# Optimization experiments

Hardware: AMD Instinct MI355X
Metric: run time of the kernel (lower is better)

## Reference

```python
import jax, jax.numpy as jnp
import numpy as np

DIM = 512
HEADS = 4
MARGIN = 1.0


def _attn_pool(x, Wq, bq, Wk, bk, Wv, bv, Wo, bo):
    # SelfAttention(video_dim, m_dim=DIM, heads=HEADS) followed by mean over time
    B, T, _ = x.shape
    hd = DIM // HEADS
    q = (x @ Wq + bq).reshape(B, T, HEADS, hd)
    k = (x @ Wk + bk).reshape(B, T, HEADS, hd)
    v = (x @ Wv + bv).reshape(B, T, HEADS, hd)
    a = jax.nn.softmax(jnp.einsum('bthd,bshd->bhts', q, k) / jnp.sqrt(jnp.float32(hd)), axis=-1)
    out = jnp.einsum('bhts,bshd->bthd', a, v).reshape(B, T, DIM) @ Wo + bo
    return out.mean(axis=1)  # [B, DIM]


def _ranking(x1, x2, gmask, margin):
    # vectorized form of the per-row torch.roll loop:
    # s[i, b] = <x1[b], x2[(b - i) mod B]>
    B = x1.shape[0]
    idx = (jnp.arange(B)[None, :] - jnp.arange(B)[:, None]) % B  # [B, B]
    s = jnp.einsum('bc,ibc->ib', x1, x2[idx])                    # [B, B]
    mask = gmask[idx] & gmask[None, :]                           # [B, B]
    # max-margin ranking loss with per-column masked mean, then mean over valid cols
    loss = jnp.maximum(0.0, margin + s[1:] - s[0:1])             # [B-1, B]
    m = mask[1:]
    cnt = m.sum(axis=0)
    col_mean = jnp.where(cnt > 0, (loss * m).sum(axis=0) / jnp.maximum(cnt, 1), 0.0)
    valid = cnt > 0
    loss_val = jnp.sum(col_mean * valid) / jnp.maximum(valid.sum(), 1)
    # ranking accuracy: idx==0 iff the true (row 0) score is max among selected
    sel_sum = jnp.sum(jnp.where(mask, s, 0.0), axis=0)
    col_valid = (sel_sum != 0) & mask.any(axis=0)
    s_masked = jnp.where(mask, s, -jnp.inf)
    top_is_first = (s[0] >= s_masked.max(axis=0)).astype(jnp.float32)
    acc = jnp.sum(jnp.where(col_valid, top_is_first, 0.0)) / jnp.maximum(col_valid.sum(), 1)
    return loss_val, jax.lax.stop_gradient(acc)


def setup_inputs() -> dict:
    key = jax.random.key(0)
    ks = iter(jax.random.split(key, 64))

    def nrm(shape, s=0.02):
        return jax.random.normal(next(ks), shape, jnp.float32) * s

    inp = {
        'o': jax.random.normal(next(ks), (128, 1024, DIM), jnp.float32),
        'rgb': jax.random.normal(next(ks), (128, 64, 2048), jnp.float32),
        'audio': jax.random.normal(next(ks), (128, 64, 128), jnp.float32),
        'group_mask': jax.random.randint(next(ks), (128,), 0, 2).astype(bool),
    }
    for name, d in (('rgb', 2048), ('audio', 128)):
        inp[f'{name}_Wq'] = nrm((d, DIM)); inp[f'{name}_bq'] = jnp.zeros((DIM,), jnp.float32)
        inp[f'{name}_Wk'] = nrm((d, DIM)); inp[f'{name}_bk'] = jnp.zeros((DIM,), jnp.float32)
        inp[f'{name}_Wv'] = nrm((d, DIM)); inp[f'{name}_bv'] = jnp.zeros((DIM,), jnp.float32)
        inp[f'{name}_Wo'] = nrm((DIM, DIM)); inp[f'{name}_bo'] = jnp.zeros((DIM,), jnp.float32)
        inp[f'{name}_W2'] = nrm((DIM, DIM)); inp[f'{name}_b2'] = jnp.zeros((DIM,), jnp.float32)
    inp['expand_W'] = nrm((DIM, 2 * DIM))
    inp['expand_b'] = jnp.zeros((2 * DIM,), jnp.float32)
    return inp


def reference(o, rgb, audio, group_mask,
              rgb_Wq, rgb_bq, rgb_Wk, rgb_bk, rgb_Wv, rgb_bv, rgb_Wo, rgb_bo, rgb_W2, rgb_b2,
              audio_Wq, audio_bq, audio_Wk, audio_bk, audio_Wv, audio_bv, audio_Wo, audio_bo,
              audio_W2, audio_b2, expand_W, expand_b):
    # per-modality encoders (CollaborativeGating multiplies are discarded in the
    # original forward, so gating is a no-op on the output -> skipped)
    f_rgb = _attn_pool(rgb, rgb_Wq, rgb_bq, rgb_Wk, rgb_bk, rgb_Wv, rgb_bv, rgb_Wo, rgb_bo) @ rgb_W2 + rgb_b2
    f_aud = _attn_pool(audio, audio_Wq, audio_bq, audio_Wk, audio_bk, audio_Wv, audio_bv, audio_Wo, audio_bo) @ audio_W2 + audio_b2
    feat = jnp.concatenate([f_rgb, f_aud], axis=-1)  # [B, 2*DIM]
    oo = o.mean(axis=-2) @ expand_W + expand_b       # [B, 2*DIM]
    oo = oo / jnp.maximum(jnp.linalg.norm(oo, axis=-1, keepdims=True), 1e-12)
    l1, a1 = _ranking(oo, feat, group_mask, MARGIN)
    l2, a2 = _ranking(feat, oo, group_mask, MARGIN)
    loss = l1 + l2
    acc = (a1 + a2) / 2.0
    return loss, acc
```

## Files before the change

kernel.cpp:

```cpp
#include <hip/hip_runtime.h>
#include <hip/hip_bf16.h>
#include <math.h>


using bf16x8 = __attribute__((ext_vector_type(8))) __bf16;
using f32x4  = __attribute__((ext_vector_type(4))) float;

enum : size_t {
  B_PART = 0,
  B_OM   = B_PART + (size_t)128*16*2*512*4,
  B_OO   = B_OM   + (size_t)128*512*4,
  B_G    = B_OO   + (size_t)128*1024*4,
  B_PP   = B_G    + (size_t)128*128*4,
  B_PO   = B_PP   + (size_t)2*128*512*4,
  B_FEAT = B_PO   + (size_t)2*128*512*4,
  B_QBF  = B_FEAT + (size_t)2*128*512*4,
  B_KBF  = B_QBF  + (size_t)2*8192*512*2,
  B_VBF  = B_KBF  + (size_t)2*8192*512*2,
  B_XR   = B_VBF  + (size_t)2*8192*512*2,
  B_XA   = B_XR   + (size_t)8192*2048*2,
  B_WT   = B_XA   + (size_t)8192*128*2,
  B_END  = B_WT   + (size_t)3*512*2048*2 + (size_t)3*512*128*2
};

__device__ __forceinline__ unsigned short f2bf(float f) {
  __hip_bfloat16 h = __float2bfloat16(f);
  return __builtin_bit_cast(unsigned short, h);
}
__device__ __forceinline__ unsigned pack2(float a, float b) {
  return (unsigned)f2bf(a) | ((unsigned)f2bf(b) << 16);
}

struct PrepArgs {
  const float* xr; unsigned short* xrb;
  const float* xa; unsigned short* xab;
  const float* w[6];
  unsigned short* wt[6];
};

__device__ __forceinline__ void castT64(const float* __restrict__ W,
                                        unsigned short* __restrict__ Wt,
                                        int K, int n0, int k0, int tid) {
  __shared__ float t[64][65];
  int c = tid & 63, r4 = tid >> 6;
#pragma unroll
  for (int i = 0; i < 16; ++i) {
    int r = r4 * 16 + i;
    t[c][r] = W[(size_t)(k0 + r) * 512 + n0 + c];
  }
  __syncthreads();
  int nr = tid >> 3, kk = (tid & 7) * 8;
#pragma unroll
  for (int p = 0; p < 2; ++p) {
    int n = nr + p * 32;
    float4 x0 = *(const float4*)&t[n][kk];
    float4 x1 = *(const float4*)&t[n][kk + 4];
    uint4 pk;
    pk.x = pack2(x0.x, x0.y); pk.y = pack2(x0.z, x0.w);
    pk.z = pack2(x1.x, x1.y); pk.w = pack2(x1.z, x1.w);
    *(uint4*)&Wt[(size_t)(n0 + n) * K + k0 + kk] = pk;
  }
}

__device__ __forceinline__ void cast8(const float* __restrict__ x,
                                      unsigned short* __restrict__ y,
                                      int i, int stride, int total) {
  for (; i < total; i += stride) {
    float4 v0 = *(const float4*)(x + (size_t)i * 8);
    float4 v1 = *(const float4*)(x + (size_t)i * 8 + 4);
    uint4 pk;
    pk.x = pack2(v0.x, v0.y); pk.y = pack2(v0.z, v0.w);
    pk.z = pack2(v1.x, v1.y); pk.w = pack2(v1.z, v1.w);
    *(uint4*)(y + (size_t)i * 8) = pk;
  }
}

__global__ __launch_bounds__(256) void prep_k(PrepArgs a) {
  int bid = blockIdx.x, tid = threadIdx.x;
  if (bid < 768) {
    int w = bid >> 8, t = bid & 255;
    castT64(a.w[w], a.wt[w], 2048, (t >> 5) * 64, (t & 31) * 64, tid);
  } else if (bid < 816) {
    int t = bid - 768; int w = t >> 4; t &= 15;
    castT64(a.w[3 + w], a.wt[3 + w], 128, (t >> 1) * 64, (t & 1) * 64, tid);
  } else if (bid < 1840) {
    cast8(a.xr, a.xrb, (bid - 816) * 256 + tid, 262144, 2097152);
  } else {
    cast8(a.xa, a.xab, (bid - 1840) * 256 + tid, 16384, 131072);
  }
}

struct QkvAll {
  const unsigned short* A[2];
  const unsigned short* Wt[6];
  const float* bias[6];
  unsigned short* out[6];
  const float* o; float* part;
};

__device__ __forceinline__ void stage16(const void* g, void* l) {
  __builtin_amdgcn_global_load_lds((const __attribute__((address_space(1))) void*)g,
                                   (__attribute__((address_space(3))) void*)l, 16, 0, 0);
}

__global__ __launch_bounds__(256) void qkv_mean_k(QkvAll args) {
  __shared__ __align__(16) char smem[49152];

  int id = blockIdx.x;
  int blk = id / 448, off = id % 448;

  if (off >= 192) {
    int mb = blk * 256 + (off - 192);
    int c = mb & 15, b = mb >> 4;
    const float* base = args.o + ((size_t)b * 1024 + (size_t)c * 64) * 512;
    int tid = threadIdx.x;
    int d4 = (tid & 127) << 2, half = tid >> 7;
    float4 s = {0.f, 0.f, 0.f, 0.f};
    for (int t = half; t < 64; t += 2) {
      float4 v = *(const float4*)(base + (size_t)t * 512 + d4);
      s.x += v.x; s.y += v.y; s.z += v.z; s.w += v.w;
    }
    *(float4*)(args.part + (((size_t)b * 16 + c) * 2 + half) * 512 + d4) = s;
    return;
  }

  int qid = blk * 192 + off;
  int mi = qid >= 768 ? 1 : 0; qid -= mi * 768;
  int by = qid & 63, bx = (qid >> 6) & 3, bz = qid >> 8;
  int K = mi ? 128 : 2048;
  int nt = K >> 5;
  const unsigned short* A = args.A[mi];
  int wi = mi * 3 + bz;
  const unsigned short* Bt = args.Wt[wi];
  const float* bias = args.bias[wi];

  int tid = threadIdx.x;
  int l = tid & 63, w = tid >> 6;
  int row0 = by * 128, col0 = bx * 128;
  int wrow = (w & 1) * 64, wcol = (w >> 1) * 64;
  int kg = l >> 4, lr = l & 15;

  float bv[4];
#pragma unroll
  for (int n = 0; n < 4; ++n) bv[n] = bias[col0 + wcol + n * 16 + lr];
  asm volatile("" :: "v"(bv[0]), "v"(bv[1]), "v"(bv[2]), "v"(bv[3]));

  auto stage_pair = [&](char* dbuf, int k0s) {
#pragma unroll
    for (int i = 0; i < 2; ++i) {
      int c = w * 128 + i * 64 + l;
      int B_ = c << 4;
      int e6 = ((B_ >> 6) ^ (B_ >> 8)) & 1;
      int E  = B_ ^ (e6 << 4) ^ (((B_ >> 7) & 1) << 5) ^ (((B_ >> 8) & 1) << 6);
      int r = E >> 6, s = ((E >> 4) & 3) << 3;
      stage16(A + (size_t)(row0 + r) * K + k0s + s, dbuf + (w * 128 + i * 64) * 16);
      stage16(Bt + (size_t)(col0 + r) * K + k0s + s, dbuf + 8192 + (w * 128 + i * 64) * 16);
    }
  };

  f32x4 acc[4][4] = {};
  int xorA = (lr & 15 & 7) << 4;

  stage_pair(smem, 0);
  if (nt > 1) stage_pair(smem + 16384, 32);
  int cur = 0;
  for (int t = 0; t < nt; ++t) {
    if (t + 1 < nt) {
      asm volatile("s_waitcnt vmcnt(4)" ::: "memory");
    } else {
      asm volatile("s_waitcnt vmcnt(0)" ::: "memory");
    }
    __builtin_amdgcn_s_barrier();
    __builtin_amdgcn_sched_barrier(0);

    if (t + 2 < nt) {
      int nb = cur + 2; if (nb >= 3) nb -= 3;
      stage_pair(smem + nb * 16384, (t + 2) << 5);
    }

    const char* Ab = smem + cur * 16384;
    const char* Bb = Ab + 8192;
    bf16x8 af[4], bfr[4];
#pragma unroll
    for (int m = 0; m < 4; ++m) {
      int ra = wrow + m * 16 + lr;
      int rb = wcol + m * 16 + lr;
      af[m]  = *(const bf16x8*)(Ab + (((ra << 6) + (kg << 4)) ^ xorA));
      bfr[m] = *(const bf16x8*)(Bb + (((rb << 6) + (kg << 4)) ^ xorA));
    }
#pragma unroll
    for (int m = 0; m < 4; ++m)
#pragma unroll
      for (int n = 0; n < 4; ++n)
        acc[m][n] = __builtin_amdgcn_mfma_f32_16x16x32_bf16(af[m], bfr[n], acc[m][n], 0, 0, 0);

    __builtin_amdgcn_sched_barrier(0);
    cur += 1; if (cur >= 3) cur = 0;
  }

  __syncthreads();

  float* cst = (float*)(smem) + w * 1024;
  unsigned short* C = args.out[wi];
  int rr = l >> 3, q = l & 7;
#pragma unroll
  for (int m = 0; m < 4; ++m) {
#pragma unroll
    for (int n = 0; n < 4; ++n) {
      int g0 = (n * 16 + lr) >> 3, o0 = lr & 7;
#pragma unroll
      for (int j = 0; j < 4; ++j) {
        int row = kg * 4 + j;
        cst[row * 64 + (((g0 ^ (row & 7)) << 3) | o0)] = acc[m][n][j] + bv[n];
      }
    }
#pragma unroll
    for (int p = 0; p < 2; ++p) {
      int row = rr + p * 8;
      int grp = q ^ (row & 7);
      float4 x0 = *(const float4*)&cst[row * 64 + grp * 8];
      float4 x1 = *(const float4*)&cst[row * 64 + grp * 8 + 4];
      uint4 pk;
      pk.x = pack2(x0.x, x0.y); pk.y = pack2(x0.z, x0.w);
      pk.z = pack2(x1.x, x1.y); pk.w = pack2(x1.z, x1.w);
      *(uint4*)&C[(size_t)(row0 + wrow + m * 16 + row) * 512 + col0 + wcol + q * 8] = pk;
    }
  }
}

__global__ __launch_bounds__(512) void finalize_mean_k(const float* __restrict__ part,
                                                       float* __restrict__ om) {
  int b = blockIdx.x, d = threadIdx.x;
  float s = 0.f;
  for (int c = 0; c < 32; ++c) s += part[((size_t)b * 32 + c) * 512 + d];
  om[(size_t)b * 512 + d] = s * (1.f / 1024.f);
}

__global__ __launch_bounds__(256) void gemm_f32_k(
    const float* __restrict__ A, int lda,
    const float* __restrict__ W, int ldw,
    const float* __restrict__ bias,
    float* __restrict__ C, int ldc, int K) {
  __shared__ float As[16][65];
  __shared__ float Ws[16][64];
  int tid = threadIdx.x;
  int tx = tid & 15, ty = tid >> 4;
  int row0 = blockIdx.y * 64, col0 = blockIdx.x * 64;
  float acc[4][4] = {};
  int ar = tid >> 2, ac = (tid & 3) << 2;
  int wr = tid >> 4, wc = (tid & 15) << 2;
  for (int k0 = 0; k0 < K; k0 += 16) {
    float4 av = *(const float4*)(A + (size_t)(row0 + ar) * lda + k0 + ac);
    As[ac + 0][ar] = av.x; As[ac + 1][ar] = av.y;
    As[ac + 2][ar] = av.z; As[ac + 3][ar] = av.w;
    float4 wv = *(const float4*)(W + (size_t)(k0 + wr) * ldw + col0 + wc);
    *(float4*)&Ws[wr][wc] = wv;
    __syncthreads();
#pragma unroll
    for (int k = 0; k < 16; ++k) {
      float a0 = As[k][(ty << 2) + 0], a1 = As[k][(ty << 2) + 1];
      float a2 = As[k][(ty << 2) + 2], a3 = As[k][(ty << 2) + 3];
      float4 w = *(const float4*)&Ws[k][tx << 2];
      acc[0][0] += a0 * w.x; acc[0][1] += a0 * w.y; acc[0][2] += a0 * w.z; acc[0][3] += a0 * w.w;
      acc[1][0] += a1 * w.x; acc[1][1] += a1 * w.y; acc[1][2] += a1 * w.z; acc[1][3] += a1 * w.w;
      acc[2][0] += a2 * w.x; acc[2][1] += a2 * w.y; acc[2][2] += a2 * w.z; acc[2][3] += a2 * w.w;
      acc[3][0] += a3 * w.x; acc[3][1] += a3 * w.y; acc[3][2] += a3 * w.z; acc[3][3] += a3 * w.w;
    }
    __syncthreads();
  }
  float4 bv = *(const float4*)(bias + col0 + (tx << 2));
#pragma unroll
  for (int i = 0; i < 4; ++i) {
    float4 ov;
    ov.x = acc[i][0] + bv.x; ov.y = acc[i][1] + bv.y;
    ov.z = acc[i][2] + bv.z; ov.w = acc[i][3] + bv.w;
    *(float4*)(C + (size_t)(row0 + (ty << 2) + i) * ldc + col0 + (tx << 2)) = ov;
  }
}

__global__ __launch_bounds__(256) void gemm_f32_2w_k(
    const float* __restrict__ A,
    const float* __restrict__ W0, const float* __restrict__ W1,
    const float* __restrict__ b0, const float* __restrict__ b1,
    float* __restrict__ C) {
  const float* W = (blockIdx.y >= 2) ? W1 : W0;
  const float* bias = (blockIdx.y >= 2) ? b1 : b0;
  __shared__ float As[16][65];
  __shared__ float Ws[16][64];
  int tid = threadIdx.x;
  int tx = tid & 15, ty = tid >> 4;
  int row0 = blockIdx.y * 64, col0 = blockIdx.x * 64;
  float acc[4][4] = {};
  int ar = tid >> 2, ac = (tid & 3) << 2;
  int wr = tid >> 4, wc = (tid & 15) << 2;
  for (int k0 = 0; k0 < 512; k0 += 16) {
    float4 av = *(const float4*)(A + (size_t)(row0 + ar) * 512 + k0 + ac);
    As[ac + 0][ar] = av.x; As[ac + 1][ar] = av.y;
    As[ac + 2][ar] = av.z; As[ac + 3][ar] = av.w;
    float4 wv = *(const float4*)(W + (size_t)(k0 + wr) * 512 + col0 + wc);
    *(float4*)&Ws[wr][wc] = wv;
    __syncthreads();
#pragma unroll
    for (int k = 0; k < 16; ++k) {
      float a0 = As[k][(ty << 2) + 0], a1 = As[k][(ty << 2) + 1];
      float a2 = As[k][(ty << 2) + 2], a3 = As[k][(ty << 2) + 3];
      float4 w = *(const float4*)&Ws[k][tx << 2];
      acc[0][0] += a0 * w.x; acc[0][1] += a0 * w.y; acc[0][2] += a0 * w.z; acc[0][3] += a0 * w.w;
      acc[1][0] += a1 * w.x; acc[1][1] += a1 * w.y; acc[1][2] += a1 * w.z; acc[1][3] += a1 * w.w;
      acc[2][0] += a2 * w.x; acc[2][1] += a2 * w.y; acc[2][2] += a2 * w.z; acc[2][3] += a2 * w.w;
      acc[3][0] += a3 * w.x; acc[3][1] += a3 * w.y; acc[3][2] += a3 * w.z; acc[3][3] += a3 * w.w;
    }
    __syncthreads();
  }
  float4 bv = *(const float4*)(bias + col0 + (tx << 2));
#pragma unroll
  for (int i = 0; i < 4; ++i) {
    float4 ov;
    ov.x = acc[i][0] + bv.x; ov.y = acc[i][1] + bv.y;
    ov.z = acc[i][2] + bv.z; ov.w = acc[i][3] + bv.w;
    *(float4*)(C + (size_t)(row0 + (ty << 2) + i) * 512 + col0 + (tx << 2)) = ov;
  }
}

__global__ __launch_bounds__(256) void attn_pool_k(
    const unsigned short* __restrict__ qbf,
    const unsigned short* __restrict__ kbf,
    const unsigned short* __restrict__ vbf,
    float* __restrict__ pooled) {
  __shared__ float wlds[4][64];
  int b = blockIdx.x, m = blockIdx.y;
  int tid = threadIdx.x;
  int w = tid >> 6, l = tid & 63, lr = l & 15, g = l >> 4;
  size_t base = ((size_t)m * 8192 + (size_t)b * 64) * 512 + w * 128;

  bf16x8 qf[4][4];
#pragma unroll
  for (int tb = 0; tb < 4; ++tb)
#pragma unroll
    for (int ks = 0; ks < 4; ++ks)
      qf[tb][ks] = *(const bf16x8*)(qbf + base + (size_t)(tb * 16 + lr) * 512 + ks * 32 + g * 8);

  f32x4 acc[4][4] = {};
#pragma unroll
  for (int sb = 0; sb < 4; ++sb) {
    bf16x8 kf[4];
#pragma unroll
    for (int ks = 0; ks < 4; ++ks)
      kf[ks] = *(const bf16x8*)(kbf + base + (size_t)(sb * 16 + lr) * 512 + ks * 32 + g * 8);
#pragma unroll
    for (int tb = 0; tb < 4; ++tb)
#pragma unroll
      for (int ks = 0; ks < 4; ++ks)
        acc[sb][tb] = __builtin_amdgcn_mfma_f32_16x16x32_bf16(kf[ks], qf[tb][ks], acc[sb][tb], 0, 0, 0);
  }

  const float scale = 0.08838834764831845f;
  float mx[4] = {-INFINITY, -INFINITY, -INFINITY, -INFINITY};
#pragma unroll
  for (int sb = 0; sb < 4; ++sb)
#pragma unroll
    for (int tb = 0; tb < 4; ++tb)
#pragma unroll
      for (int j = 0; j < 4; ++j) {
        acc[sb][tb][j] *= scale;
        mx[tb] = fmaxf(mx[tb], acc[sb][tb][j]);
      }
#pragma unroll
  for (int tb = 0; tb < 4; ++tb) {
    mx[tb] = fmaxf(mx[tb], __shfl_xor(mx[tb], 16));
    mx[tb] = fmaxf(mx[tb], __shfl_xor(mx[tb], 32));
  }
  float sm[4] = {0.f, 0.f, 0.f, 0.f};
#pragma unroll
  for (int sb = 0; sb < 4; ++sb)
#pragma unroll
    for (int tb = 0; tb < 4; ++tb)
#pragma unroll
      for (int j = 0; j < 4; ++j) {
        float e = expf(acc[sb][tb][j] - mx[tb]);
        acc[sb][tb][j] = e;
        sm[tb] += e;
      }
  float inv[4];
#pragma unroll
  for (int tb = 0; tb < 4; ++tb) {
    sm[tb] += __shfl_xor(sm[tb], 16);
    sm[tb] += __shfl_xor(sm[tb], 32);
    inv[tb] = 1.f / sm[tb];
  }
#pragma unroll
  for (int sb = 0; sb < 4; ++sb)
#pragma unroll
    for (int j = 0; j < 4; ++j) {
      float cs = acc[sb][0][j] * inv[0] + acc[sb][1][j] * inv[1]
               + acc[sb][2][j] * inv[2] + acc[sb][3][j] * inv[3];
      cs += __shfl_xor(cs, 1);
      cs += __shfl_xor(cs, 2);
      cs += __shfl_xor(cs, 4);
      cs += __shfl_xor(cs, 8);
      if (lr == 0) wlds[w][sb * 16 + g * 4 + j] = cs * (1.f / 64.f);
    }
  __syncthreads();

  int h = tid >> 6, c2 = (tid & 63) << 1;
  size_t vbase = ((size_t)m * 8192 + (size_t)b * 64) * 512 + h * 128 + c2;
  float s0 = 0.f, s1 = 0.f;
#pragma unroll 8
  for (int s = 0; s < 64; ++s) {
    unsigned u = *(const unsigned*)(vbf + vbase + (size_t)s * 512);
    float vlo = __builtin_bit_cast(float, u << 16);
    float vhi = __builtin_bit_cast(float, u & 0xffff0000u);
    float wv = wlds[h][s];
    s0 += wv * vlo; s1 += wv * vhi;
  }
  float2 o2 = {s0, s1};
  *(float2*)(pooled + ((size_t)m * 128 + b) * 512 + h * 128 + c2) = o2;
}

__global__ __launch_bounds__(256) void ntg_k(const float* __restrict__ oo,
                                             const float* __restrict__ feat,
                                             float* __restrict__ G) {
  __shared__ float As[16][33], Bs[16][33];
  __shared__ float inv32[32];
  int tid = threadIdx.x;
  int row0 = blockIdx.y * 32, col0 = blockIdx.x * 32;
  int ar = tid >> 3, aq = tid & 7;
  int ty = tid >> 4, tx = tid & 15;
  float acc[2][2] = {};
  float ssq = 0.f;
  for (int k0 = 0; k0 < 1024; k0 += 16) {
    float2 av = *(const float2*)(oo + (size_t)(row0 + ar) * 1024 + k0 + aq * 2);
    As[aq * 2 + 0][ar] = av.x;
    As[aq * 2 + 1][ar] = av.y;
    ssq += av.x * av.x + av.y * av.y;
    int kk = k0 + aq * 2;
    float2 bv = *(const float2*)(feat + (size_t)((kk >> 9) * 128 + col0 + ar) * 512 + (kk & 511));
    Bs[aq * 2 + 0][ar] = bv.x;
    Bs[aq * 2 + 1][ar] = bv.y;
    __syncthreads();
#pragma unroll
    for (int k = 0; k < 16; ++k) {
      float a0 = As[k][ty * 2], a1 = As[k][ty * 2 + 1];
      float b0 = Bs[k][tx * 2], b1 = Bs[k][tx * 2 + 1];
      acc[0][0] += a0 * b0; acc[0][1] += a0 * b1;
      acc[1][0] += a1 * b0; acc[1][1] += a1 * b1;
    }
    __syncthreads();
  }
  ssq += __shfl_xor(ssq, 1);
  ssq += __shfl_xor(ssq, 2);
  ssq += __shfl_xor(ssq, 4);
  if (aq == 0) inv32[ar] = 1.f / fmaxf(sqrtf(ssq), 1e-12f);
  __syncthreads();
#pragma unroll
  for (int i = 0; i < 2; ++i)
#pragma unroll
    for (int j = 0; j < 2; ++j)
      G[(size_t)(row0 + ty * 2 + i) * 128 + col0 + tx * 2 + j] = acc[i][j] * inv32[ty * 2 + i];
}

__global__ __launch_bounds__(128) void final_k(const float* __restrict__ G,
                                               const int* __restrict__ gmask,
                                               float* __restrict__ out) {
  __shared__ float cm[2][128], vd[2][128], tp[2][128], cv[2][128];
  __shared__ int gm[128];
  int b = threadIdx.x;
  gm[b] = gmask[b];
  __syncthreads();
  for (int r = 0; r < 2; ++r) {
    bool gb = gm[b] != 0;
    float s0 = G[b * 128 + b];
    int cnt = 0;
    float lsum = 0.f, selsum = 0.f, smax = -INFINITY;
    bool anym = false;
    for (int i = 0; i < 128; ++i) {
      int j = (b - i + 128) & 127;
      bool mk = gb && (gm[j] != 0);
      float sv = (r == 0) ? G[b * 128 + j] : G[j * 128 + b];
      if (mk) {
        selsum += sv; anym = true;
        smax = fmaxf(smax, sv);
        if (i >= 1) { cnt++; lsum += fmaxf(0.f, 1.f + sv - s0); }
      }
    }
    cm[r][b] = (cnt > 0) ? (lsum / (float)cnt) : 0.f;
    vd[r][b] = (cnt > 0) ? 1.f : 0.f;
    bool colvalid = (selsum != 0.f) && anym;
    tp[r][b] = (colvalid && (s0 >= smax)) ? 1.f : 0.f;
    cv[r][b] = colvalid ? 1.f : 0.f;
  }
  __syncthreads();
  if (b == 0) {
    float loss = 0.f, acc = 0.f;
    for (int r = 0; r < 2; ++r) {
      float scm = 0, svd = 0, stp = 0, scv = 0;
      for (int i = 0; i < 128; ++i) { scm += cm[r][i]; svd += vd[r][i]; stp += tp[r][i]; scv += cv[r][i]; }
      loss += scm / fmaxf(svd, 1.f);
      acc += stp / fmaxf(scv, 1.f);
    }
    out[0] = loss;
    out[1] = acc * 0.5f;
  }
}

extern "C" void kernel_launch(void* const* d_in, const int* in_sizes, int n_in,
                              void* d_out, int out_size, void* d_ws, size_t ws_size,
                              hipStream_t stream) {
  const float* o     = (const float*)d_in[0];
  const float* rgb   = (const float*)d_in[1];
  const float* audio = (const float*)d_in[2];
  const int* gmask   = (const int*)d_in[3];
  const float* W[2][10];
  for (int m = 0; m < 2; ++m)
    for (int w = 0; w < 10; ++w) W[m][w] = (const float*)d_in[4 + m * 10 + w];
  const float* expand_W = (const float*)d_in[24];
  const float* expand_b = (const float*)d_in[25];

  char* ws = (char*)d_ws;
  float* part = (float*)(ws + B_PART);
  float* om   = (float*)(ws + B_OM);
  float* oo   = (float*)(ws + B_OO);
  float* G    = (float*)(ws + B_G);
  float* pp2  = (float*)(ws + B_PP);
  float* po2  = (float*)(ws + B_PO);
  float* feat2= (float*)(ws + B_FEAT);
  unsigned short* qbf = (unsigned short*)(ws + B_QBF);
  unsigned short* kbf = (unsigned short*)(ws + B_KBF);
  unsigned short* vbf = (unsigned short*)(ws + B_VBF);
  unsigned short* xrb = (unsigned short*)(ws + B_XR);
  unsigned short* xab = (unsigned short*)(ws + B_XA);
  unsigned short* wt  = (unsigned short*)(ws + B_WT);
  unsigned short* wtp[6];
  wtp[0] = wt;
  wtp[1] = wtp[0] + (size_t)512 * 2048;
  wtp[2] = wtp[1] + (size_t)512 * 2048;
  wtp[3] = wtp[2] + (size_t)512 * 2048;
  wtp[4] = wtp[3] + (size_t)512 * 128;
  wtp[5] = wtp[4] + (size_t)512 * 128;

  PrepArgs pa;
  pa.xr = rgb;   pa.xrb = xrb;
  pa.xa = audio; pa.xab = xab;
  pa.w[0] = W[0][0]; pa.w[1] = W[0][2]; pa.w[2] = W[0][4];
  pa.w[3] = W[1][0]; pa.w[4] = W[1][2]; pa.w[5] = W[1][4];
  for (int i = 0; i < 6; ++i) pa.wt[i] = wtp[i];
  prep_k<<<1904, 256, 0, stream>>>(pa);

  QkvAll qa;
  qa.A[0] = xrb; qa.A[1] = xab;
  for (int i = 0; i < 6; ++i) qa.Wt[i] = wtp[i];
  qa.bias[0] = W[0][1]; qa.bias[1] = W[0][3]; qa.bias[2] = W[0][5];
  qa.bias[3] = W[1][1]; qa.bias[4] = W[1][3]; qa.bias[5] = W[1][5];
  qa.out[0] = qbf;                       qa.out[1] = kbf;                       qa.out[2] = vbf;
  qa.out[3] = qbf + (size_t)8192 * 512;  qa.out[4] = kbf + (size_t)8192 * 512;  qa.out[5] = vbf + (size_t)8192 * 512;
  qa.o = o; qa.part = part;
  qkv_mean_k<<<3584, 256, 0, stream>>>(qa);

  finalize_mean_k<<<128, 512, 0, stream>>>(part, om);
  gemm_f32_k<<<dim3(16, 2), 256, 0, stream>>>(om, 512, expand_W, 1024, expand_b, oo, 1024, 512);

  attn_pool_k<<<dim3(128, 2), 256, 0, stream>>>(qbf, kbf, vbf, pp2);

  gemm_f32_2w_k<<<dim3(8, 4), 256, 0, stream>>>(pp2, W[0][6], W[1][6], W[0][7], W[1][7], po2);
  gemm_f32_2w_k<<<dim3(8, 4), 256, 0, stream>>>(po2, W[0][8], W[1][8], W[0][9], W[1][9], feat2);

  ntg_k<<<dim3(4, 4), 256, 0, stream>>>(oo, feat2, G);
  final_k<<<1, 128, 0, stream>>>(G, gmask, (float*)d_out);
}
```

Measured before the change: 383.6 us.

## Fuse tail kernels into one persistent kernel with grid-wide barriers

Seven small tail launches (mean finalize, expand GEMM, attention pooling, two projection GEMMs, score matrix, final loss) are merged into a single 256-block kernel. The stages are separated by a software grid barrier built on global atomics, and the barrier counter is reset in the prep kernel. This removes per-launch overhead and the idle gaps between tiny dependent kernels. In exchange it adds spin-wait barrier cost and relies on all 256 blocks being resident at once.

```diff
diff --git a/kernel.cpp b/kernel.cpp
--- a/kernel.cpp
+++ b/kernel.cpp
@@ -20,7 +20,8 @@
   B_XR   = B_VBF  + (size_t)2*8192*512*2,
   B_XA   = B_XR   + (size_t)8192*2048*2,
   B_WT   = B_XA   + (size_t)8192*128*2,
-  B_END  = B_WT   + (size_t)3*512*2048*2 + (size_t)3*512*128*2
+  B_BAR  = B_WT   + (size_t)3*512*2048*2 + (size_t)3*512*128*2,
+  B_END  = B_BAR + 64
 };
 
 __device__ __forceinline__ unsigned short f2bf(float f) {
@@ -29,6 +30,24 @@
 }
 __device__ __forceinline__ unsigned pack2(float a, float b) {
   return (unsigned)f2bf(a) | ((unsigned)f2bf(b) << 16);
+}
+
+__device__ __forceinline__ void gsync(unsigned* bar) {
+  __syncthreads();
+  if (threadIdx.x == 0) {
+    __threadfence();
+    unsigned g = __hip_atomic_load(bar + 1, __ATOMIC_RELAXED, __HIP_MEMORY_SCOPE_AGENT);
+    unsigned a = __hip_atomic_fetch_add(bar, 1u, __ATOMIC_ACQ_REL, __HIP_MEMORY_SCOPE_AGENT);
+    if (a == 255u) {
+      __hip_atomic_store(bar, 0u, __ATOMIC_RELAXED, __HIP_MEMORY_SCOPE_AGENT);
+      __hip_atomic_fetch_add(bar + 1, 1u, __ATOMIC_ACQ_REL, __HIP_MEMORY_SCOPE_AGENT);
+    } else {
+      while (__hip_atomic_load(bar + 1, __ATOMIC_ACQUIRE, __HIP_MEMORY_SCOPE_AGENT) == g)
+        __builtin_amdgcn_s_sleep(1);
+    }
+    __threadfence();
+  }
+  __syncthreads();
 }
 
 struct PrepArgs {
@@ -36,6 +55,7 @@
   const float* xa; unsigned short* xab;
   const float* w[6];
   unsigned short* wt[6];
+  unsigned* bar;
 };
 
 __device__ __forceinline__ void castT64(const float* __restrict__ W,
@@ -77,6 +97,8 @@
 
 __global__ __launch_bounds__(256) void prep_k(PrepArgs a) {
   int bid = blockIdx.x, tid = threadIdx.x;
+  if (bid == 0 && tid == 0)
+    __hip_atomic_store(a.bar, 0u, __ATOMIC_RELAXED, __HIP_MEMORY_SCOPE_AGENT);
   if (bid < 768) {
     int w = bid >> 8, t = bid & 255;
     castT64(a.w[w], a.wt[w], 2048, (t >> 5) * 64, (t & 31) * 64, tid);
@@ -159,7 +181,7 @@
   };
 
   f32x4 acc[4][4] = {};
-  int xorA = (lr & 15 & 7) << 4;
+  int xorA = (lr & 7) << 4;
 
   stage_pair(smem, 0);
   if (nt > 1) stage_pair(smem + 16384, 32);
@@ -228,24 +250,105 @@
   }
 }
 
-__global__ __launch_bounds__(512) void finalize_mean_k(const float* __restrict__ part,
-                                                       float* __restrict__ om) {
-  int b = blockIdx.x, d = threadIdx.x;
-  float s = 0.f;
-  for (int c = 0; c < 32; ++c) s += part[((size_t)b * 32 + c) * 512 + d];
-  om[(size_t)b * 512 + d] = s * (1.f / 1024.f);
-}
-
-__global__ __launch_bounds__(256) void gemm_f32_k(
-    const float* __restrict__ A, int lda,
-    const float* __restrict__ W, int ldw,
-    const float* __restrict__ bias,
-    float* __restrict__ C, int ldc, int K) {
+__device__ void attn_dev(const unsigned short* qbf, const unsigned short* kbf,
+                         const unsigned short* vbf, float* pooled, int b, int m) {
+  __shared__ float wlds[4][64];
+  int tid = threadIdx.x;
+  int w = tid >> 6, l = tid & 63, lr = l & 15, g = l >> 4;
+  size_t base = ((size_t)m * 8192 + (size_t)b * 64) * 512 + w * 128;
+
+  bf16x8 qf[4][4];
+#pragma unroll
+  for (int tb = 0; tb < 4; ++tb)
+#pragma unroll
+    for (int ks = 0; ks < 4; ++ks)
+      qf[tb][ks] = *(const bf16x8*)(qbf + base + (size_t)(tb * 16 + lr) * 512 + ks * 32 + g * 8);
+
+  f32x4 acc[4][4] = {};
+#pragma unroll
+  for (int sb = 0; sb < 4; ++sb) {
+    bf16x8 kf[4];
+#pragma unroll
+    for (int ks = 0; ks < 4; ++ks)
+      kf[ks] = *(const bf16x8*)(kbf + base + (size_t)(sb * 16 + lr) * 512 + ks * 32 + g * 8);
+#pragma unroll
+    for (int tb = 0; tb < 4; ++tb)
+#pragma unroll
+      for (int ks = 0; ks < 4; ++ks)
+        acc[sb][tb] = __builtin_amdgcn_mfma_f32_16x16x32_bf16(kf[ks], qf[tb][ks], acc[sb][tb], 0, 0, 0);
+  }
+
+  const float scale = 0.08838834764831845f;
+  float mx[4] = {-INFINITY, -INFINITY, -INFINITY, -INFINITY};
+#pragma unroll
+  for (int sb = 0; sb < 4; ++sb)
+#pragma unroll
+    for (int tb = 0; tb < 4; ++tb)
+#pragma unroll
+      for (int j = 0; j < 4; ++j) {
+        acc[sb][tb][j] *= scale;
+        mx[tb] = fmaxf(mx[tb], acc[sb][tb][j]);
+      }
+#pragma unroll
+  for (int tb = 0; tb < 4; ++tb) {
+    mx[tb] = fmaxf(mx[tb], __shfl_xor(mx[tb], 16));
+    mx[tb] = fmaxf(mx[tb], __shfl_xor(mx[tb], 32));
+  }
+  float sm[4] = {0.f, 0.f, 0.f, 0.f};
+#pragma unroll
+  for (int sb = 0; sb < 4; ++sb)
+#pragma unroll
+    for (int tb = 0; tb < 4; ++tb)
+#pragma unroll
+      for (int j = 0; j < 4; ++j) {
+        float e = expf(acc[sb][tb][j] - mx[tb]);
+        acc[sb][tb][j] = e;
+        sm[tb] += e;
+      }
+  float inv[4];
+#pragma unroll
+  for (int tb = 0; tb < 4; ++tb) {
+    sm[tb] += __shfl_xor(sm[tb], 16);
+    sm[tb] += __shfl_xor(sm[tb], 32);
+    inv[tb] = 1.f / sm[tb];
+  }
+#pragma unroll
+  for (int sb = 0; sb < 4; ++sb)
+#pragma unroll
+    for (int j = 0; j < 4; ++j) {
+      float cs = acc[sb][0][j] * inv[0] + acc[sb][1][j] * inv[1]
+               + acc[sb][2][j] * inv[2] + acc[sb][3][j] * inv[3];
+      cs += __shfl_xor(cs, 1);
+      cs += __shfl_xor(cs, 2);
+      cs += __shfl_xor(cs, 4);
+      cs += __shfl_xor(cs, 8);
+      if (lr == 0) wlds[w][sb * 16 + g * 4 + j] = cs * (1.f / 64.f);
+    }
+  __syncthreads();
+
+  int h = tid >> 6, c2 = (tid & 63) << 1;
+  size_t vbase = ((size_t)m * 8192 + (size_t)b * 64) * 512 + h * 128 + c2;
+  float s0 = 0.f, s1 = 0.f;
+#pragma unroll 8
+  for (int s = 0; s < 64; ++s) {
+    unsigned u = *(const unsigned*)(vbf + vbase + (size_t)s * 512);
+    float vlo = __builtin_bit_cast(float, u << 16);
+    float vhi = __builtin_bit_cast(float, u & 0xffff0000u);
+    float wv = wlds[h][s];
+    s0 += wv * vlo; s1 += wv * vhi;
+  }
+  float2 o2 = {s0, s1};
+  *(float2*)(pooled + ((size_t)m * 128 + b) * 512 + h * 128 + c2) = o2;
+}
+
+__device__ void gemm_dev(const float* A, int lda, const float* W, int ldw,
+                         const float* bias, float* C, int ldc, int K,
+                         int bx, int by) {
   __shared__ float As[16][65];
   __shared__ float Ws[16][64];
   int tid = threadIdx.x;
   int tx = tid & 15, ty = tid >> 4;
-  int row0 = blockIdx.y * 64, col0 = blockIdx.x * 64;
+  int row0 = by * 64, col0 = bx * 64;
   float acc[4][4] = {};
   int ar = tid >> 2, ac = (tid & 3) << 2;
   int wr = tid >> 4, wc = (tid & 15) << 2;
@@ -278,152 +381,12 @@
   }
 }
 
-__global__ __launch_bounds__(256) void gemm_f32_2w_k(
-    const float* __restrict__ A,
-    const float* __restrict__ W0, const float* __restrict__ W1,
-    const float* __restrict__ b0, const float* __restrict__ b1,
-    float* __restrict__ C) {
-  const float* W = (blockIdx.y >= 2) ? W1 : W0;
-  const float* bias = (blockIdx.y >= 2) ? b1 : b0;
-  __shared__ float As[16][65];
-  __shared__ float Ws[16][64];
-  int tid = threadIdx.x;
-  int tx = tid & 15, ty = tid >> 4;
-  int row0 = blockIdx.y * 64, col0 = blockIdx.x * 64;
-  float acc[4][4] = {};
-  int ar = tid >> 2, ac = (tid & 3) << 2;
-  int wr = tid >> 4, wc = (tid & 15) << 2;
-  for (int k0 = 0; k0 < 512; k0 += 16) {
-    float4 av = *(const float4*)(A + (size_t)(row0 + ar) * 512 + k0 + ac);
-    As[ac + 0][ar] = av.x; As[ac + 1][ar] = av.y;
-    As[ac + 2][ar] = av.z; As[ac + 3][ar] = av.w;
-    float4 wv = *(const float4*)(W + (size_t)(k0 + wr) * 512 + col0 + wc);
-    *(float4*)&Ws[wr][wc] = wv;
-    __syncthreads();
-#pragma unroll
-    for (int k = 0; k < 16; ++k) {
-      float a0 = As[k][(ty << 2) + 0], a1 = As[k][(ty << 2) + 1];
-      float a2 = As[k][(ty << 2) + 2], a3 = As[k][(ty << 2) + 3];
-      float4 w = *(const float4*)&Ws[k][tx << 2];
-      acc[0][0] += a0 * w.x; acc[0][1] += a0 * w.y; acc[0][2] += a0 * w.z; acc[0][3] += a0 * w.w;
-      acc[1][0] += a1 * w.x; acc[1][1] += a1 * w.y; acc[1][2] += a1 * w.z; acc[1][3] += a1 * w.w;
-      acc[2][0] += a2 * w.x; acc[2][1] += a2 * w.y; acc[2][2] += a2 * w.z; acc[2][3] += a2 * w.w;
-      acc[3][0] += a3 * w.x; acc[3][1] += a3 * w.y; acc[3][2] += a3 * w.z; acc[3][3] += a3 * w.w;
-    }
-    __syncthreads();
-  }
-  float4 bv = *(const float4*)(bias + col0 + (tx << 2));
-#pragma unroll
-  for (int i = 0; i < 4; ++i) {
-    float4 ov;
-    ov.x = acc[i][0] + bv.x; ov.y = acc[i][1] + bv.y;
-    ov.z = acc[i][2] + bv.z; ov.w = acc[i][3] + bv.w;
-    *(float4*)(C + (size_t)(row0 + (ty << 2) + i) * 512 + col0 + (tx << 2)) = ov;
-  }
-}
-
-__global__ __launch_bounds__(256) void attn_pool_k(
-    const unsigned short* __restrict__ qbf,
-    const unsigned short* __restrict__ kbf,
-    const unsigned short* __restrict__ vbf,
-    float* __restrict__ pooled) {
-  __shared__ float wlds[4][64];
-  int b = blockIdx.x, m = blockIdx.y;
-  int tid = threadIdx.x;
-  int w = tid >> 6, l = tid & 63, lr = l & 15, g = l >> 4;
-  size_t base = ((size_t)m * 8192 + (size_t)b * 64) * 512 + w * 128;
-
-  bf16x8 qf[4][4];
-#pragma unroll
-  for (int tb = 0; tb < 4; ++tb)
-#pragma unroll
-    for (int ks = 0; ks < 4; ++ks)
-      qf[tb][ks] = *(const bf16x8*)(qbf + base + (size_t)(tb * 16 + lr) * 512 + ks * 32 + g * 8);
-
-  f32x4 acc[4][4] = {};
-#pragma unroll
-  for (int sb = 0; sb < 4; ++sb) {
-    bf16x8 kf[4];
-#pragma unroll
-    for (int ks = 0; ks < 4; ++ks)
-      kf[ks] = *(const bf16x8*)(kbf + base + (size_t)(sb * 16 + lr) * 512 + ks * 32 + g * 8);
-#pragma unroll
-    for (int tb = 0; tb < 4; ++tb)
-#pragma unroll
-      for (int ks = 0; ks < 4; ++ks)
-        acc[sb][tb] = __builtin_amdgcn_mfma_f32_16x16x32_bf16(kf[ks], qf[tb][ks], acc[sb][tb], 0, 0, 0);
-  }
-
-  const float scale = 0.08838834764831845f;
-  float mx[4] = {-INFINITY, -INFINITY, -INFINITY, -INFINITY};
-#pragma unroll
-  for (int sb = 0; sb < 4; ++sb)
-#pragma unroll
-    for (int tb = 0; tb < 4; ++tb)
-#pragma unroll
-      for (int j = 0; j < 4; ++j) {
-        acc[sb][tb][j] *= scale;
-        mx[tb] = fmaxf(mx[tb], acc[sb][tb][j]);
-      }
-#pragma unroll
-  for (int tb = 0; tb < 4; ++tb) {
-    mx[tb] = fmaxf(mx[tb], __shfl_xor(mx[tb], 16));
-    mx[tb] = fmaxf(mx[tb], __shfl_xor(mx[tb], 32));
-  }
-  float sm[4] = {0.f, 0.f, 0.f, 0.f};
-#pragma unroll
-  for (int sb = 0; sb < 4; ++sb)
-#pragma unroll
-    for (int tb = 0; tb < 4; ++tb)
-#pragma unroll
-      for (int j = 0; j < 4; ++j) {
-        float e = expf(acc[sb][tb][j] - mx[tb]);
-        acc[sb][tb][j] = e;
-        sm[tb] += e;
-      }
-  float inv[4];
-#pragma unroll
-  for (int tb = 0; tb < 4; ++tb) {
-    sm[tb] += __shfl_xor(sm[tb], 16);
-    sm[tb] += __shfl_xor(sm[tb], 32);
-    inv[tb] = 1.f / sm[tb];
-  }
-#pragma unroll
-  for (int sb = 0; sb < 4; ++sb)
-#pragma unroll
-    for (int j = 0; j < 4; ++j) {
-      float cs = acc[sb][0][j] * inv[0] + acc[sb][1][j] * inv[1]
-               + acc[sb][2][j] * inv[2] + acc[sb][3][j] * inv[3];
-      cs += __shfl_xor(cs, 1);
-      cs += __shfl_xor(cs, 2);
-      cs += __shfl_xor(cs, 4);
-      cs += __shfl_xor(cs, 8);
-      if (lr == 0) wlds[w][sb * 16 + g * 4 + j] = cs * (1.f / 64.f);
-    }
-  __syncthreads();
-
-  int h = tid >> 6, c2 = (tid & 63) << 1;
-  size_t vbase = ((size_t)m * 8192 + (size_t)b * 64) * 512 + h * 128 + c2;
-  float s0 = 0.f, s1 = 0.f;
-#pragma unroll 8
-  for (int s = 0; s < 64; ++s) {
-    unsigned u = *(const unsigned*)(vbf + vbase + (size_t)s * 512);
-    float vlo = __builtin_bit_cast(float, u << 16);
-    float vhi = __builtin_bit_cast(float, u & 0xffff0000u);
-    float wv = wlds[h][s];
-    s0 += wv * vlo; s1 += wv * vhi;
-  }
-  float2 o2 = {s0, s1};
-  *(float2*)(pooled + ((size_t)m * 128 + b) * 512 + h * 128 + c2) = o2;
-}
-
-__global__ __launch_bounds__(256) void ntg_k(const float* __restrict__ oo,
-                                             const float* __restrict__ feat,
-                                             float* __restrict__ G) {
+__device__ void ntg_dev(const float* oo, const float* feat, float* G,
+                        int bx, int by) {
   __shared__ float As[16][33], Bs[16][33];
   __shared__ float inv32[32];
   int tid = threadIdx.x;
-  int row0 = blockIdx.y * 32, col0 = blockIdx.x * 32;
+  int row0 = by * 32, col0 = bx * 32;
   int ar = tid >> 3, aq = tid & 7;
   int ty = tid >> 4, tx = tid & 15;
   float acc[2][2] = {};
@@ -459,35 +422,35 @@
       G[(size_t)(row0 + ty * 2 + i) * 128 + col0 + tx * 2 + j] = acc[i][j] * inv32[ty * 2 + i];
 }
 
-__global__ __launch_bounds__(128) void final_k(const float* __restrict__ G,
-                                               const int* __restrict__ gmask,
-                                               float* __restrict__ out) {
+__device__ void final_dev(const float* G, const int* gmask, float* out) {
   __shared__ float cm[2][128], vd[2][128], tp[2][128], cv[2][128];
   __shared__ int gm[128];
   int b = threadIdx.x;
-  gm[b] = gmask[b];
-  __syncthreads();
-  for (int r = 0; r < 2; ++r) {
-    bool gb = gm[b] != 0;
-    float s0 = G[b * 128 + b];
-    int cnt = 0;
-    float lsum = 0.f, selsum = 0.f, smax = -INFINITY;
-    bool anym = false;
-    for (int i = 0; i < 128; ++i) {
-      int j = (b - i + 128) & 127;
-      bool mk = gb && (gm[j] != 0);
-      float sv = (r == 0) ? G[b * 128 + j] : G[j * 128 + b];
-      if (mk) {
-        selsum += sv; anym = true;
-        smax = fmaxf(smax, sv);
-        if (i >= 1) { cnt++; lsum += fmaxf(0.f, 1.f + sv - s0); }
+  if (b < 128) gm[b] = gmask[b];
+  __syncthreads();
+  if (b < 128) {
+    for (int r = 0; r < 2; ++r) {
+      bool gb = gm[b] != 0;
+      float s0 = G[b * 128 + b];
+      int cnt = 0;
+      float lsum = 0.f, selsum = 0.f, smax = -INFINITY;
+      bool anym = false;
+      for (int i = 0; i < 128; ++i) {
+        int j = (b - i + 128) & 127;
+        bool mk = gb && (gm[j] != 0);
+        float sv = (r == 0) ? G[b * 128 + j] : G[j * 128 + b];
+        if (mk) {
+          selsum += sv; anym = true;
+          smax = fmaxf(smax, sv);
+          if (i >= 1) { cnt++; lsum += fmaxf(0.f, 1.f + sv - s0); }
+        }
       }
-    }
-    cm[r][b] = (cnt > 0) ? (lsum / (float)cnt) : 0.f;
-    vd[r][b] = (cnt > 0) ? 1.f : 0.f;
-    bool colvalid = (selsum != 0.f) && anym;
-    tp[r][b] = (colvalid && (s0 >= smax)) ? 1.f : 0.f;
-    cv[r][b] = colvalid ? 1.f : 0.f;
+      cm[r][b] = (cnt > 0) ? (lsum / (float)cnt) : 0.f;
+      vd[r][b] = (cnt > 0) ? 1.f : 0.f;
+      bool colvalid = (selsum != 0.f) && anym;
+      tp[r][b] = (colvalid && (s0 >= smax)) ? 1.f : 0.f;
+      cv[r][b] = colvalid ? 1.f : 0.f;
+    }
   }
   __syncthreads();
   if (b == 0) {
@@ -501,6 +464,55 @@
     out[0] = loss;
     out[1] = acc * 0.5f;
   }
+}
+
+struct TailArgs {
+  const float* part; float* om;
+  const float* expand_W; const float* expand_b; float* oo;
+  const unsigned short* qbf; const unsigned short* kbf; const unsigned short* vbf;
+  float* pp;
+  const float* Wo[2]; const float* bo[2];
+  const float* W2[2]; const float* b2[2];
+  float* po; float* feat;
+  float* G; const int* gmask; float* out;
+  unsigned* bar;
+};
+
+__global__ __launch_bounds__(256) void tail_k(TailArgs a) {
+  int blk = blockIdx.x, tid = threadIdx.x;
+
+  if (blk < 128) {
+    for (int d = tid; d < 512; d += 256) {
+      float s = 0.f;
+      for (int c = 0; c < 32; ++c) s += a.part[((size_t)blk * 32 + c) * 512 + d];
+      a.om[(size_t)blk * 512 + d] = s * (1.f / 1024.f);
+    }
+  }
+  attn_dev(a.qbf, a.kbf, a.vbf, a.pp, blk & 127, blk >> 7);
+  gsync(a.bar);
+
+  if (blk < 32) {
+    gemm_dev(a.om, 512, a.expand_W, 1024, a.expand_b, a.oo, 1024, 512,
+             blk & 15, blk >> 4);
+  } else if (blk < 64) {
+    int t = blk - 32;
+    int by = t >> 3, bx = t & 7;
+    int m = by >> 1;
+    gemm_dev(a.pp, 512, a.Wo[m], 512, a.bo[m], a.po, 512, 512, bx, by);
+  }
+  gsync(a.bar);
+
+  if (blk < 32) {
+    int by = blk >> 3, bx = blk & 7;
+    int m = by >> 1;
+    gemm_dev(a.po, 512, a.W2[m], 512, a.b2[m], a.feat, 512, 512, bx, by);
+  }
+  gsync(a.bar);
+
+  if (blk < 16) ntg_dev(a.oo, a.feat, a.G, blk & 3, blk >> 2);
+  gsync(a.bar);
+
+  if (blk == 0) final_dev(a.G, a.gmask, a.out);
 }
 
 extern "C" void kernel_launch(void* const* d_in, const int* in_sizes, int n_in,
@@ -530,6 +542,7 @@
   unsigned short* xrb = (unsigned short*)(ws + B_XR);
   unsigned short* xab = (unsigned short*)(ws + B_XA);
   unsigned short* wt  = (unsigned short*)(ws + B_WT);
+  unsigned* bar = (unsigned*)(ws + B_BAR);
   unsigned short* wtp[6];
   wtp[0] = wt;
   wtp[1] = wtp[0] + (size_t)512 * 2048;
@@ -544,6 +557,7 @@
   pa.w[0] = W[0][0]; pa.w[1] = W[0][2]; pa.w[2] = W[0][4];
   pa.w[3] = W[1][0]; pa.w[4] = W[1][2]; pa.w[5] = W[1][4];
   for (int i = 0; i < 6; ++i) pa.wt[i] = wtp[i];
+  pa.bar = bar;
   prep_k<<<1904, 256, 0, stream>>>(pa);
 
   QkvAll qa;
@@ -556,14 +570,15 @@
   qa.o = o; qa.part = part;
   qkv_mean_k<<<3584, 256, 0, stream>>>(qa);
 
-  finalize_mean_k<<<128, 512, 0, stream>>>(part, om);
-  gemm_f32_k<<<dim3(16, 2), 256, 0, stream>>>(om, 512, expand_W, 1024, expand_b, oo, 1024, 512);
-
-  attn_pool_k<<<dim3(128, 2), 256, 0, stream>>>(qbf, kbf, vbf, pp2);
-
-  gemm_f32_2w_k<<<dim3(8, 4), 256, 0, stream>>>(pp2, W[0][6], W[1][6], W[0][7], W[1][7], po2);
-  gemm_f32_2w_k<<<dim3(8, 4), 256, 0, stream>>>(po2, W[0][8], W[1][8], W[0][9], W[1][9], feat2);
-
-  ntg_k<<<dim3(4, 4), 256, 0, stream>>>(oo, feat2, G);
-  final_k<<<1, 128, 0, stream>>>(G, gmask, (float*)d_out);
-}
+  TailArgs ta;
+  ta.part = part; ta.om = om;
+  ta.expand_W = expand_W; ta.expand_b = expand_b; ta.oo = oo;
+  ta.qbf = qbf; ta.kbf = kbf; ta.vbf = vbf;
+  ta.pp = pp2;
+  ta.Wo[0] = W[0][6]; ta.bo[0] = W[0][7]; ta.W2[0] = W[0][8]; ta.b2[0] = W[0][9];
+  ta.Wo[1] = W[1][6]; ta.bo[1] = W[1][7]; ta.W2[1] = W[1][8]; ta.b2[1] = W[1][9];
+  ta.po = po2; ta.feat = feat2;
+  ta.G = G; ta.gmask = gmask; ta.out = (float*)d_out;
+  ta.bar = bar;
+  tail_k<<<256, 256, 0, stream>>>(ta);
+}
```

New measurement: 634.8 us. 1.65x slower.
